# Kernel tuning notes

Hardware: AMD Instinct MI355X
Metric: run time of the kernel (lower is better)

## Reference

```python
import jax, jax.numpy as jnp
import numpy as np

B, C, HID, H, W = 32, 1024, 512, 56, 56

def setup_inputs() -> dict:
    key = jax.random.key(0)
    ks = jax.random.split(key, 8)
    s = 0.02
    return {
        "x":  jax.random.normal(ks[0], (B, C, H, W), dtype=jnp.float32),
        "W1": jax.random.normal(ks[1], (C, HID), dtype=jnp.float32) * s,  # mlp Linear(C->hidden), no bias
        "W2": jax.random.normal(ks[2], (HID, C), dtype=jnp.float32) * s,  # mlp Linear(hidden->C), no bias
        "WA": jax.random.normal(ks[3], (C, H), dtype=jnp.float32) * s,    # fc_A weight (transposed)
        "bA": jax.random.normal(ks[4], (H,), dtype=jnp.float32) * s,
        "WB": jax.random.normal(ks[5], (C, W), dtype=jnp.float32) * s,    # fc_B weight (transposed)
        "bB": jax.random.normal(ks[6], (W,), dtype=jnp.float32) * s,
    }

def reference(x, W1, W2, WA, bA, WB, bB):
    # Global average pool over spatial dims: (B, C)
    y = jnp.mean(x, axis=(2, 3))
    # MLP with exact (erf) GELU; dropout is identity in eval mode
    h = jax.nn.gelu(y @ W1, approximate=False)          # (B, HID)
    yp = jax.nn.gelu(h @ W2, approximate=False)          # (B, C)
    # Original replicates yp across C channels before fc_A/fc_B, so every
    # channel's attention map is identical: compute once, broadcast.
    A = yp @ WA + bA                                     # (B, H)
    Bv = yp @ WB + bB                                    # (B, W)
    attn = jax.nn.sigmoid(A[:, None, :, None] * Bv[:, None, None, :])  # (B, 1, H, W)
    return jnp.broadcast_to(attn, (x.shape[0], x.shape[1], A.shape[1], Bv.shape[1]))
```

## Files before the change

kernel.cpp:

```cpp
#include <hip/hip_runtime.h>
#include <math.h>

#define BATCH 32
#define NC    1024
#define NHID  512
#define NH    56
#define NW    56
#define HWSZ  3136
#define HW4   784

typedef float nfloat4 __attribute__((ext_vector_type(4)));

__device__ __forceinline__ float gelu_exact(float x) {
    return 0.5f * x * (1.0f + erff(x * 0.7071067811865476f));
}

__global__ __launch_bounds__(256) void gap_kernel(const float* __restrict__ x,
                                                  float* __restrict__ y) {
    const int row  = (blockIdx.x << 2) | (threadIdx.x >> 6);
    const int lane = threadIdx.x & 63;
    const float4* xr = (const float4*)(x + (size_t)row * HWSZ);

    float s = 0.f;
#pragma unroll
    for (int it = 0; it < 12; ++it) {
        float4 v = xr[lane + (it << 6)];
        s += (v.x + v.y) + (v.z + v.w);
    }
    if (lane < 16) {
        float4 v = xr[768 + lane];
        s += (v.x + v.y) + (v.z + v.w);
    }
#pragma unroll
    for (int off = 32; off > 0; off >>= 1) s += __shfl_down(s, off);
    if (lane == 0) y[row] = s * (1.0f / 3136.0f);
}

__global__ __launch_bounds__(256) void fc1_kernel(const float* __restrict__ y,
                                                  const float* __restrict__ W1,
                                                  float* __restrict__ h) {
    const int jc = blockIdx.x;
    const int b  = blockIdx.y;
    const int t  = threadIdx.x;

    __shared__ float sy[NC];
    __shared__ float part[256];
    for (int i = t; i < NC; i += 256) sy[i] = y[b * NC + i];
    __syncthreads();

    const int j  = jc * 64 + (t & 63);
    const int ks = (t >> 6) * 256;
    const float* w = W1 + (size_t)ks * NHID + j;

    float a0 = 0.f, a1 = 0.f, a2 = 0.f, a3 = 0.f;
    for (int c = 0; c < 256; c += 4) {
        a0 += sy[ks + c + 0] * w[(size_t)(c + 0) * NHID];
        a1 += sy[ks + c + 1] * w[(size_t)(c + 1) * NHID];
        a2 += sy[ks + c + 2] * w[(size_t)(c + 2) * NHID];
        a3 += sy[ks + c + 3] * w[(size_t)(c + 3) * NHID];
    }
    part[t] = (a0 + a1) + (a2 + a3);
    __syncthreads();
    if (t < 64) {
        float v = part[t] + part[t + 64] + part[t + 128] + part[t + 192];
        h[b * NHID + jc * 64 + t] = gelu_exact(v);
    }
}

__global__ __launch_bounds__(256) void fc2_kernel(const float* __restrict__ h,
                                                  const float* __restrict__ W2,
                                                  float* __restrict__ yp) {
    const int cc = blockIdx.x;
    const int b  = blockIdx.y;
    const int t  = threadIdx.x;

    __shared__ float sh[NHID];
    __shared__ float part[256];
    for (int i = t; i < NHID; i += 256) sh[i] = h[b * NHID + i];
    __syncthreads();

    const int c  = cc * 64 + (t & 63);
    const int js = (t >> 6) * 128;
    const float* w = W2 + (size_t)js * NC + c;

    float a0 = 0.f, a1 = 0.f, a2 = 0.f, a3 = 0.f;
    for (int jj = 0; jj < 128; jj += 4) {
        a0 += sh[js + jj + 0] * w[(size_t)(jj + 0) * NC];
        a1 += sh[js + jj + 1] * w[(size_t)(jj + 1) * NC];
        a2 += sh[js + jj + 2] * w[(size_t)(jj + 2) * NC];
        a3 += sh[js + jj + 3] * w[(size_t)(jj + 3) * NC];
    }
    part[t] = (a0 + a1) + (a2 + a3);
    __syncthreads();
    if (t < 64) {
        float v = part[t] + part[t + 64] + part[t + 128] + part[t + 192];
        yp[b * NC + cc * 64 + t] = gelu_exact(v);
    }
}

__global__ __launch_bounds__(256) void ab_kernel(
    const float* __restrict__ yp, const float* __restrict__ WA,
    const float* __restrict__ bA, const float* __restrict__ WB,
    const float* __restrict__ bB, float* __restrict__ AB) {
    const int b = blockIdx.x;
    const int t = threadIdx.x;

    __shared__ float sp[NC];
    __shared__ float partA[256];
    __shared__ float partB[256];
    for (int i = t; i < NC; i += 256) sp[i] = yp[b * NC + i];
    __syncthreads();

    const int i  = t & 63;
    const int ks = (t >> 6) * 256;
    float a0 = 0.f, a1 = 0.f, a2 = 0.f, a3 = 0.f;
    float b0 = 0.f, b1 = 0.f, b2 = 0.f, b3 = 0.f;
    if (i < NH) {
        const float* wa = WA + (size_t)ks * NH + i;
        const float* wb = WB + (size_t)ks * NW + i;
        for (int c = 0; c < 256; c += 4) {
            a0 += sp[ks + c + 0] * wa[(size_t)(c + 0) * NH];
            a1 += sp[ks + c + 1] * wa[(size_t)(c + 1) * NH];
            a2 += sp[ks + c + 2] * wa[(size_t)(c + 2) * NH];
            a3 += sp[ks + c + 3] * wa[(size_t)(c + 3) * NH];
            b0 += sp[ks + c + 0] * wb[(size_t)(c + 0) * NW];
            b1 += sp[ks + c + 1] * wb[(size_t)(c + 1) * NW];
            b2 += sp[ks + c + 2] * wb[(size_t)(c + 2) * NW];
            b3 += sp[ks + c + 3] * wb[(size_t)(c + 3) * NW];
        }
    }
    partA[t] = (a0 + a1) + (a2 + a3);
    partB[t] = (b0 + b1) + (b2 + b3);
    __syncthreads();
    if (t < NH) {
        AB[b * 128 + t] = bA[t] + partA[t] + partA[t + 64] + partA[t + 128] + partA[t + 192];
        AB[b * 128 + 64 + t] = bB[t] + partB[t] + partB[t + 64] + partB[t + 128] + partB[t + 192];
    }
}

__global__ __launch_bounds__(256) void bcast_kernel(const float* __restrict__ AB,
                                                    float* __restrict__ out) {
    const int blk = blockIdx.x;
    const int b = blk >> 6;
    const int cchunk = blk & 63;
    const int t = threadIdx.x;

    __shared__ float sA[NH];
    __shared__ float sB[NW];
    if (t < NH) sA[t] = AB[b * 128 + t];
    else if (t >= 64 && t < 64 + NW) sB[t - 64] = AB[b * 128 + t];
    __syncthreads();

    nfloat4 v[4];
#pragma unroll
    for (int it = 0; it < 4; ++it) {
        const int idx = t + it * 256;
        if (idx < HW4) {
            const int r  = idx / 14;
            const int cb = (idx - r * 14) * 4;
            const float a = sA[r];
            nfloat4 q;
            q.x = 1.0f / (1.0f + expf(-(a * sB[cb + 0])));
            q.y = 1.0f / (1.0f + expf(-(a * sB[cb + 1])));
            q.z = 1.0f / (1.0f + expf(-(a * sB[cb + 2])));
            q.w = 1.0f / (1.0f + expf(-(a * sB[cb + 3])));
            v[it] = q;
        }
    }

    const size_t base = ((size_t)b * NC + (size_t)cchunk * 16) * HW4;
#pragma unroll
    for (int ch = 0; ch < 16; ++ch) {
        nfloat4* orow = (nfloat4*)out + base + (size_t)ch * HW4;
#pragma unroll
        for (int it = 0; it < 4; ++it) {
            const int idx = t + it * 256;
            if (idx < HW4) __builtin_nontemporal_store(v[it], &orow[idx]);
        }
    }
}

extern "C" void kernel_launch(void* const* d_in, const int* in_sizes, int n_in,
                              void* d_out, int out_size, void* d_ws, size_t ws_size,
                              hipStream_t stream) {
    const float* x  = (const float*)d_in[0];
    const float* W1 = (const float*)d_in[1];
    const float* W2 = (const float*)d_in[2];
    const float* WA = (const float*)d_in[3];
    const float* bA = (const float*)d_in[4];
    const float* WB = (const float*)d_in[5];
    const float* bB = (const float*)d_in[6];
    float* out = (float*)d_out;

    float* y  = (float*)d_ws;
    float* yp = y;
    float* h  = y + BATCH * NC;
    float* AB = h + BATCH * NHID;

    gap_kernel<<<BATCH * NC / 4, 256, 0, stream>>>(x, y);
    fc1_kernel<<<dim3(NHID / 64, BATCH), 256, 0, stream>>>(y, W1, h);
    fc2_kernel<<<dim3(NC / 64, BATCH), 256, 0, stream>>>(h, W2, yp);
    ab_kernel<<<BATCH, 256, 0, stream>>>(yp, WA, bA, WB, bB, AB);
    bcast_kernel<<<BATCH * (NC / 16), 256, 0, stream>>>(AB, out);
}
```

Measured before the change: 181.5 us.

## Vectorize FC weight loads, nontemporal GAP loads, widen ab_kernel to 512 threads

The GAP reduction now reads x with nontemporal loads so the one-pass stream is meant to bypass cache retention. fc1 and fc2 are reorganised so each thread loads float4 weight rows and keeps vector accumulators over a shorter K slice, with a 16-way shared-memory reduction at the end. ab_kernel doubles its block size to split the K dimension eight ways. Together these aim to cut instruction count and latency in the small GEMV stages, at the cost of a longer final reduction and different summation order.

```diff
diff --git a/kernel.cpp b/kernel.cpp
--- a/kernel.cpp
+++ b/kernel.cpp
@@ -19,16 +19,16 @@
                                                   float* __restrict__ y) {
     const int row  = (blockIdx.x << 2) | (threadIdx.x >> 6);
     const int lane = threadIdx.x & 63;
-    const float4* xr = (const float4*)(x + (size_t)row * HWSZ);
+    const nfloat4* xr = (const nfloat4*)(x + (size_t)row * HWSZ);
 
     float s = 0.f;
 #pragma unroll
     for (int it = 0; it < 12; ++it) {
-        float4 v = xr[lane + (it << 6)];
+        nfloat4 v = __builtin_nontemporal_load(xr + lane + (it << 6));
         s += (v.x + v.y) + (v.z + v.w);
     }
     if (lane < 16) {
-        float4 v = xr[768 + lane];
+        nfloat4 v = __builtin_nontemporal_load(xr + 768 + lane);
         s += (v.x + v.y) + (v.z + v.w);
     }
 #pragma unroll
@@ -44,26 +44,35 @@
     const int t  = threadIdx.x;
 
     __shared__ float sy[NC];
-    __shared__ float part[256];
+    __shared__ nfloat4 part[256];
     for (int i = t; i < NC; i += 256) sy[i] = y[b * NC + i];
     __syncthreads();
 
-    const int j  = jc * 64 + (t & 63);
-    const int ks = (t >> 6) * 256;
-    const float* w = W1 + (size_t)ks * NHID + j;
-
-    float a0 = 0.f, a1 = 0.f, a2 = 0.f, a3 = 0.f;
-    for (int c = 0; c < 256; c += 4) {
-        a0 += sy[ks + c + 0] * w[(size_t)(c + 0) * NHID];
-        a1 += sy[ks + c + 1] * w[(size_t)(c + 1) * NHID];
-        a2 += sy[ks + c + 2] * w[(size_t)(c + 2) * NHID];
-        a3 += sy[ks + c + 3] * w[(size_t)(c + 3) * NHID];
-    }
-    part[t] = (a0 + a1) + (a2 + a3);
-    __syncthreads();
-    if (t < 64) {
-        float v = part[t] + part[t + 64] + part[t + 128] + part[t + 192];
-        h[b * NHID + jc * 64 + t] = gelu_exact(v);
+    const int lane4 = t & 15;
+    const int j0 = jc * 64 + lane4 * 4;
+    const int ks = (t >> 4) * 64;
+
+    nfloat4 acc0 = {0.f, 0.f, 0.f, 0.f};
+    nfloat4 acc1 = {0.f, 0.f, 0.f, 0.f};
+    const float* wbase = W1 + (size_t)ks * NHID + j0;
+#pragma unroll 8
+    for (int c = 0; c < 64; c += 2) {
+        nfloat4 w0 = *(const nfloat4*)(wbase + (size_t)(c + 0) * NHID);
+        nfloat4 w1 = *(const nfloat4*)(wbase + (size_t)(c + 1) * NHID);
+        acc0 += sy[ks + c + 0] * w0;
+        acc1 += sy[ks + c + 1] * w1;
+    }
+    part[t] = acc0 + acc1;
+    __syncthreads();
+    if (t < 16) {
+        nfloat4 s = part[t];
+#pragma unroll
+        for (int g = 1; g < 16; ++g) s += part[g * 16 + t];
+        float* hp = h + b * NHID + jc * 64 + t * 4;
+        hp[0] = gelu_exact(s.x);
+        hp[1] = gelu_exact(s.y);
+        hp[2] = gelu_exact(s.z);
+        hp[3] = gelu_exact(s.w);
     }
 }
 
@@ -75,30 +84,39 @@
     const int t  = threadIdx.x;
 
     __shared__ float sh[NHID];
-    __shared__ float part[256];
+    __shared__ nfloat4 part[256];
     for (int i = t; i < NHID; i += 256) sh[i] = h[b * NHID + i];
     __syncthreads();
 
-    const int c  = cc * 64 + (t & 63);
-    const int js = (t >> 6) * 128;
-    const float* w = W2 + (size_t)js * NC + c;
-
-    float a0 = 0.f, a1 = 0.f, a2 = 0.f, a3 = 0.f;
-    for (int jj = 0; jj < 128; jj += 4) {
-        a0 += sh[js + jj + 0] * w[(size_t)(jj + 0) * NC];
-        a1 += sh[js + jj + 1] * w[(size_t)(jj + 1) * NC];
-        a2 += sh[js + jj + 2] * w[(size_t)(jj + 2) * NC];
-        a3 += sh[js + jj + 3] * w[(size_t)(jj + 3) * NC];
-    }
-    part[t] = (a0 + a1) + (a2 + a3);
-    __syncthreads();
-    if (t < 64) {
-        float v = part[t] + part[t + 64] + part[t + 128] + part[t + 192];
-        yp[b * NC + cc * 64 + t] = gelu_exact(v);
-    }
-}
-
-__global__ __launch_bounds__(256) void ab_kernel(
+    const int lane4 = t & 15;
+    const int c0 = cc * 64 + lane4 * 4;
+    const int js = (t >> 4) * 32;
+
+    nfloat4 acc0 = {0.f, 0.f, 0.f, 0.f};
+    nfloat4 acc1 = {0.f, 0.f, 0.f, 0.f};
+    const float* wbase = W2 + (size_t)js * NC + c0;
+#pragma unroll 8
+    for (int jj = 0; jj < 32; jj += 2) {
+        nfloat4 w0 = *(const nfloat4*)(wbase + (size_t)(jj + 0) * NC);
+        nfloat4 w1 = *(const nfloat4*)(wbase + (size_t)(jj + 1) * NC);
+        acc0 += sh[js + jj + 0] * w0;
+        acc1 += sh[js + jj + 1] * w1;
+    }
+    part[t] = acc0 + acc1;
+    __syncthreads();
+    if (t < 16) {
+        nfloat4 s = part[t];
+#pragma unroll
+        for (int g = 1; g < 16; ++g) s += part[g * 16 + t];
+        float* pp = yp + b * NC + cc * 64 + t * 4;
+        pp[0] = gelu_exact(s.x);
+        pp[1] = gelu_exact(s.y);
+        pp[2] = gelu_exact(s.z);
+        pp[3] = gelu_exact(s.w);
+    }
+}
+
+__global__ __launch_bounds__(512) void ab_kernel(
     const float* __restrict__ yp, const float* __restrict__ WA,
     const float* __restrict__ bA, const float* __restrict__ WB,
     const float* __restrict__ bB, float* __restrict__ AB) {
@@ -106,19 +124,19 @@
     const int t = threadIdx.x;
 
     __shared__ float sp[NC];
-    __shared__ float partA[256];
-    __shared__ float partB[256];
-    for (int i = t; i < NC; i += 256) sp[i] = yp[b * NC + i];
+    __shared__ float partA[512];
+    __shared__ float partB[512];
+    for (int i = t; i < NC; i += 512) sp[i] = yp[b * NC + i];
     __syncthreads();
 
     const int i  = t & 63;
-    const int ks = (t >> 6) * 256;
+    const int ks = (t >> 6) * 128;
     float a0 = 0.f, a1 = 0.f, a2 = 0.f, a3 = 0.f;
     float b0 = 0.f, b1 = 0.f, b2 = 0.f, b3 = 0.f;
     if (i < NH) {
         const float* wa = WA + (size_t)ks * NH + i;
         const float* wb = WB + (size_t)ks * NW + i;
-        for (int c = 0; c < 256; c += 4) {
+        for (int c = 0; c < 128; c += 4) {
             a0 += sp[ks + c + 0] * wa[(size_t)(c + 0) * NH];
             a1 += sp[ks + c + 1] * wa[(size_t)(c + 1) * NH];
             a2 += sp[ks + c + 2] * wa[(size_t)(c + 2) * NH];
@@ -133,8 +151,14 @@
     partB[t] = (b0 + b1) + (b2 + b3);
     __syncthreads();
     if (t < NH) {
-        AB[b * 128 + t] = bA[t] + partA[t] + partA[t + 64] + partA[t + 128] + partA[t + 192];
-        AB[b * 128 + 64 + t] = bB[t] + partB[t] + partB[t + 64] + partB[t + 128] + partB[t + 192];
+        float sa = bA[t], sb = bB[t];
+#pragma unroll
+        for (int g = 0; g < 8; ++g) {
+            sa += partA[g * 64 + t];
+            sb += partB[g * 64 + t];
+        }
+        AB[b * 128 + t] = sa;
+        AB[b * 128 + 64 + t] = sb;
     }
 }
 
@@ -200,6 +224,6 @@
     gap_kernel<<<BATCH * NC / 4, 256, 0, stream>>>(x, y);
     fc1_kernel<<<dim3(NHID / 64, BATCH), 256, 0, stream>>>(y, W1, h);
     fc2_kernel<<<dim3(NC / 64, BATCH), 256, 0, stream>>>(h, W2, yp);
-    ab_kernel<<<BATCH, 256, 0, stream>>>(yp, WA, bA, WB, bB, AB);
+    ab_kernel<<<BATCH, 512, 0, stream>>>(yp, WA, bA, WB, bB, AB);
     bcast_kernel<<<BATCH * (NC / 16), 256, 0, stream>>>(AB, out);
 }
```

Result: faster. 162.5 us (-10.5%).
